# Performance work log

Measured on AMD Instinct MI355X. Metric: run time of the kernel, lower is better.

Reference implementation:

```python
import jax, jax.numpy as jnp
import numpy as np

KP_VARIANCE = 0.01  # init kwarg: kp_variance (float -> plain Gaussian branch)


def make_coordinate_grid(h, w, dtype):
    # torch make_coordinate_grid: x,y in [-1,1], last dim is (x, y)
    x = jnp.linspace(-1.0, 1.0, w, dtype=dtype)
    y = jnp.linspace(-1.0, 1.0, h, dtype=dtype)
    gx, gy = jnp.meshgrid(x, y)  # each (h, w)
    return jnp.stack([gx, gy], axis=-1)  # (h, w, 2)


def grid_sample_bilinear(img, coords):
    """F.grid_sample, bilinear, zeros padding, align_corners=True.
    img: (bs, C, H, W); coords: (bs, d, K, h, w, 2) with (x, y) in [-1,1].
    Returns (bs, d, K, C, h, w)."""
    bs, C, H, W = img.shape
    x = (coords[..., 0] + 1.0) * (W - 1) / 2.0
    y = (coords[..., 1] + 1.0) * (H - 1) / 2.0
    x0 = jnp.floor(x); y0 = jnp.floor(y)
    x1 = x0 + 1.0;     y1 = y0 + 1.0
    wx1 = x - x0; wx0 = 1.0 - wx1
    wy1 = y - y0; wy0 = 1.0 - wy1

    def corner(ix, iy, wgt):
        valid = (ix >= 0) & (ix <= W - 1) & (iy >= 0) & (iy <= H - 1)
        ixc = jnp.clip(ix, 0, W - 1).astype(jnp.int32)
        iyc = jnp.clip(iy, 0, H - 1).astype(jnp.int32)
        # per-batch gather: im (C,H,W), yy/xx (d,K,h,w) -> (C,d,K,h,w)
        vals = jax.vmap(lambda im, yy, xx: im[:, yy, xx])(img, iyc, ixc)  # (bs,C,d,K,h,w)
        w_eff = (wgt * valid.astype(img.dtype))[:, None]  # (bs,1,d,K,h,w)
        return vals * w_eff

    out = (corner(x0, y0, wx0 * wy0) + corner(x1, y0, wx1 * wy0)
           + corner(x0, y1, wx0 * wy1) + corner(x1, y1, wx1 * wy1))
    return jnp.transpose(out, (0, 2, 3, 1, 4, 5))  # (bs,d,K,C,h,w)


def setup_inputs() -> dict:
    key = jax.random.key(0)
    k1, k2, k3 = jax.random.split(key, 3)
    bs, d, K, C, h, w = 4, 16, 10, 3, 128, 128
    kp_appearance_mean = jax.random.uniform(k1, (bs, 1, K, 2), jnp.float32) * 2.0 - 1.0
    kp_video_mean = jax.random.uniform(k2, (bs, d, K, 2), jnp.float32) * 2.0 - 1.0
    appearance_frame = jax.random.normal(k3, (bs, C, 1, h, w), jnp.float32)
    return {"kp_appearance_mean": kp_appearance_mean,
            "kp_video_mean": kp_video_mean,
            "appearance_frame": appearance_frame}


def reference(kp_appearance_mean, kp_video_mean, appearance_frame):
    bs, C, _, h, w = appearance_frame.shape
    _, d, K, _ = kp_video_mean.shape
    dtype = appearance_frame.dtype

    # combine_kp (difference_type='absolute', float kp_variance)
    diff = kp_video_mean - kp_video_mean[:, 0:1]          # (bs,d,K,2)
    kp_mean = diff + kp_appearance_mean                    # (bs,d,K,2)
    kp_video_diff = -diff                                  # (bs,d,K,2)

    grid = make_coordinate_grid(h, w, dtype)               # (h,w,2)

    # use_heatmap: kp2gaussian then subtract first frame
    mean_sub = grid - kp_mean[:, :, :, None, None, :]      # (bs,d,K,h,w,2)
    heatmap = jnp.exp(-0.5 * jnp.sum(mean_sub * mean_sub, axis=-1) / KP_VARIANCE)
    heatmap = heatmap - heatmap[:, 0:1]
    heatmap = heatmap[:, :, :, None]                       # (bs,d,K,1,h,w)

    # use_difference: broadcast diff over spatial dims
    diff_maps = jnp.broadcast_to(kp_video_diff[:, :, :, :, None, None],
                                 (bs, d, K, 2, h, w))

    # use_deformed_appearance: grid_sample of appearance frame by shifted grid
    deformation = grid + kp_video_diff[:, :, :, None, None, :]  # (bs,d,K,h,w,2)
    img = appearance_frame[:, :, 0]                              # (bs,C,h,w)
    deformed = grid_sample_bilinear(img, deformation)            # (bs,d,K,C,h,w)

    enc = jnp.concatenate([heatmap, diff_maps, deformed], axis=3)  # (bs,d,K,1+2+C,h,w)
    enc = enc.reshape(bs, d, -1, h, w)
    return jnp.transpose(enc, (0, 2, 1, 3, 4))  # (bs, (3+C)*K, d, h, w)
```

## Files before the change

kernel.cpp:

```cpp
#include <hip/hip_runtime.h>

#define BS 4
#define DD 16
#define KK 10
#define CC 3
#define HH 128
#define WW 128
#define HW   (HH*WW)
#define CHW  (CC*HW)
#define IMG_FLOATS (BS*CHW)
#define PAD_FLOATS 24576
#define WS_NEED ((size_t)(IMG_FLOATS + 2*PAD_FLOATS) * 4)

using f4 = __attribute__((ext_vector_type(4))) float;

struct F4U { float v[4]; };

__global__ __launch_bounds__(256) void img_pad_copy(
    const float* __restrict__ img, float* __restrict__ dst)
{
    const int i = (int)(blockIdx.x * 256u + threadIdx.x) * 4;
    *(f4*)(dst + i) = *(const f4*)(img + i);
}

template<bool PADDED>
__global__ __launch_bounds__(256) void movement_embed_kernel(
    const float* __restrict__ kp_app,
    const float* __restrict__ kp_vid,
    const float* __restrict__ src,
    float* __restrict__ out)
{
    const unsigned bi  = blockIdx.x;
    const unsigned sub = bi & 15u;
    const unsigned bdk = bi >> 4;
    const unsigned k   = bdk % KK;
    const unsigned t2  = bdk / KK;
    const unsigned d   = t2 % DD;
    const unsigned b   = t2 / DD;

    const int tid = (int)threadIdx.x;
    const int xg  = tid & 31;
    const int ly  = tid >> 5;
    const int x4  = xg * 4;
    const int y   = (int)(sub * 8u) + ly;

    const float kvx  = kp_vid[((b*DD + d)*KK + k)*2 + 0];
    const float kvy  = kp_vid[((b*DD + d)*KK + k)*2 + 1];
    const float kv0x = kp_vid[((b*DD + 0)*KK + k)*2 + 0];
    const float kv0y = kp_vid[((b*DD + 0)*KK + k)*2 + 1];
    const float kax  = kp_app[(b*KK + k)*2 + 0];
    const float kay  = kp_app[(b*KK + k)*2 + 1];

    const float diffx = kvx - kv0x;
    const float diffy = kvy - kv0y;
    const float mx = diffx + kax;
    const float my = diffy + kay;
    const float vdx = -diffx;
    const float vdy = -diffy;

    const float cx = vdx * 63.5f;
    const float cy = vdy * 63.5f;
    const float fcx = floorf(cx), fcy = floorf(cy);
    const int icx = (int)fcx, icy = (int)fcy;
    const float wx1 = cx - fcx, wx0 = 1.0f - wx1;
    const float wy1 = cy - fcy, wy0 = 1.0f - wy1;

    const int r0   = y + icy;
    const int col0 = icx + x4;
    const bool rv0 = (unsigned)r0       < (unsigned)HH;
    const bool rv1 = (unsigned)(r0 + 1) < (unsigned)HH;
    bool cv[5];
#pragma unroll
    for (int e = 0; e < 5; ++e) cv[e] = (unsigned)(col0 + e) < (unsigned)WW;

    const float step = 2.0f / 127.0f;
    const float gy  = (float)y  * step - 1.0f;
    const float gx0 = (float)x4 * step - 1.0f;
    const float dy1 = gy - my, dy0 = gy - kay;
    const float dy1sq = dy1 * dy1, dy0sq = dy0 * dy0;
    float hvv[4];
#pragma unroll
    for (int j = 0; j < 4; ++j) {
        const float gx = gx0 + (float)j * step;
        const float dx1 = gx - mx, dx0 = gx - kax;
        hvv[j] = __expf(-50.0f * (dx1 * dx1 + dy1sq))
               - __expf(-50.0f * (dx0 * dx0 + dy0sq));
    }

    const size_t chs  = (size_t)DD * HW;
    const size_t base = ((((size_t)b * (KK * 6) + k * 6) * DD + d) * HH + y) * WW + (size_t)x4;

    {
        f4 H;  H.x = hvv[0]; H.y = hvv[1]; H.z = hvv[2]; H.w = hvv[3];
        *(f4*)(out + base) = H;
        f4 VX; VX.x = vdx; VX.y = vdx; VX.z = vdx; VX.w = vdx;
        *(f4*)(out + base + chs) = VX;
        f4 VY; VY.x = vdy; VY.y = vdy; VY.z = vdy; VY.w = vdy;
        *(f4*)(out + base + 2 * chs) = VY;
    }

#pragma unroll
    for (int c = 0; c < CC; ++c) {
        float a0[5], a1[5];
        if constexpr (PADDED) {
            const long idx = (long)b * CHW + (long)c * HW + (long)r0 * WW + (long)col0;
            const float* p = src + idx;
            const F4U A  = *(const F4U*)p;
            const float a4 = p[4];
            const F4U Bt = *(const F4U*)(p + WW);
            const float b4 = p[WW + 4];
#pragma unroll
            for (int e = 0; e < 4; ++e) { a0[e] = A.v[e]; a1[e] = Bt.v[e]; }
            a0[4] = a4; a1[4] = b4;
        } else {
            const int rc0 = min(max(r0, 0), HH - 1);
            const int rc1 = min(max(r0 + 1, 0), HH - 1);
            const int cb  = b * CHW + c * HW;
#pragma unroll
            for (int e = 0; e < 5; ++e) {
                const int cc = min(max(col0 + e, 0), WW - 1);
                a0[e] = src[cb + rc0 * WW + cc];
                a1[e] = src[cb + rc1 * WW + cc];
            }
        }
#pragma unroll
        for (int e = 0; e < 5; ++e) {
            a0[e] = (rv0 && cv[e]) ? a0[e] : 0.0f;
            a1[e] = (rv1 && cv[e]) ? a1[e] : 0.0f;
        }
        float dvv[4];
#pragma unroll
        for (int e = 0; e < 4; ++e) {
            const float h0 = wx0 * a0[e] + wx1 * a0[e + 1];
            const float h1 = wx0 * a1[e] + wx1 * a1[e + 1];
            dvv[e] = wy0 * h0 + wy1 * h1;
        }
        f4 DV; DV.x = dvv[0]; DV.y = dvv[1]; DV.z = dvv[2]; DV.w = dvv[3];
        *(f4*)(out + base + (size_t)(3 + c) * chs) = DV;
    }
}

extern "C" void kernel_launch(void* const* d_in, const int* in_sizes, int n_in,
                              void* d_out, int out_size, void* d_ws, size_t ws_size,
                              hipStream_t stream) {
    const float* kp_app = (const float*)d_in[0];
    const float* kp_vid = (const float*)d_in[1];
    const float* img    = (const float*)d_in[2];
    float* out = (float*)d_out;

    const int nblocks = BS * DD * KK * 16;

    if (d_ws != nullptr && ws_size >= WS_NEED) {
        float* wimg = (float*)d_ws;
        img_pad_copy<<<IMG_FLOATS / (256 * 4), 256, 0, stream>>>(img, wimg + PAD_FLOATS);
        movement_embed_kernel<true><<<nblocks, 256, 0, stream>>>(
            kp_app, kp_vid, wimg + PAD_FLOATS, out);
    } else {
        movement_embed_kernel<false><<<nblocks, 256, 0, stream>>>(
            kp_app, kp_vid, img, out);
    }
}
```

Before: 243.9 us.

## Use persistent grid-stride sweep over contiguous output chunks, one channel per chunk

```diff
diff --git a/kernel.cpp b/kernel.cpp
--- a/kernel.cpp
+++ b/kernel.cpp
@@ -12,6 +12,11 @@
 #define PAD_FLOATS 24576
 #define WS_NEED ((size_t)(IMG_FLOATS + 2*PAD_FLOATS) * 4)
 
+#define NCH    (6*KK)
+#define NCHUNK (BS*NCH*DD*16)
+#define NBLK   2048
+#define CPB    (NCHUNK/NBLK)
+
 using f4 = __attribute__((ext_vector_type(4))) float;
 
 struct F4U { float v[4]; };
@@ -24,119 +29,114 @@
 }
 
 template<bool PADDED>
-__global__ __launch_bounds__(256) void movement_embed_kernel(
+__global__ __launch_bounds__(256) void movement_embed_sweep(
     const float* __restrict__ kp_app,
     const float* __restrict__ kp_vid,
     const float* __restrict__ src,
     float* __restrict__ out)
 {
-    const unsigned bi  = blockIdx.x;
-    const unsigned sub = bi & 15u;
-    const unsigned bdk = bi >> 4;
-    const unsigned k   = bdk % KK;
-    const unsigned t2  = bdk / KK;
-    const unsigned d   = t2 % DD;
-    const unsigned b   = t2 / DD;
+    const int tid = (int)threadIdx.x;
+    const int ly  = tid >> 5;
+    const int x4  = (tid & 31) * 4;
+    const float step = 2.0f / 127.0f;
+    const float gx0  = (float)x4 * step - 1.0f;
 
-    const int tid = (int)threadIdx.x;
-    const int xg  = tid & 31;
-    const int ly  = tid >> 5;
-    const int x4  = xg * 4;
-    const int y   = (int)(sub * 8u) + ly;
+    for (int j = (int)blockIdx.x; j < NCHUNK; j += NBLK) {
+        const int sub = j & 15;
+        const int d   = (j >> 4) & 15;
+        const unsigned bc = (unsigned)j >> 8;
+        const unsigned ch = bc % NCH;
+        const unsigned b  = bc / NCH;
+        const unsigned k  = ch / 6u;
+        const unsigned c  = ch - k * 6u;
 
-    const float kvx  = kp_vid[((b*DD + d)*KK + k)*2 + 0];
-    const float kvy  = kp_vid[((b*DD + d)*KK + k)*2 + 1];
-    const float kv0x = kp_vid[((b*DD + 0)*KK + k)*2 + 0];
-    const float kv0y = kp_vid[((b*DD + 0)*KK + k)*2 + 1];
-    const float kax  = kp_app[(b*KK + k)*2 + 0];
-    const float kay  = kp_app[(b*KK + k)*2 + 1];
+        const int y = sub * 8 + ly;
 
-    const float diffx = kvx - kv0x;
-    const float diffy = kvy - kv0y;
-    const float mx = diffx + kax;
-    const float my = diffy + kay;
-    const float vdx = -diffx;
-    const float vdy = -diffy;
+        const float kvx  = kp_vid[((b*DD + d)*KK + k)*2 + 0];
+        const float kvy  = kp_vid[((b*DD + d)*KK + k)*2 + 1];
+        const float kv0x = kp_vid[((b*DD + 0)*KK + k)*2 + 0];
+        const float kv0y = kp_vid[((b*DD + 0)*KK + k)*2 + 1];
+        const float kax  = kp_app[(b*KK + k)*2 + 0];
+        const float kay  = kp_app[(b*KK + k)*2 + 1];
 
-    const float cx = vdx * 63.5f;
-    const float cy = vdy * 63.5f;
-    const float fcx = floorf(cx), fcy = floorf(cy);
-    const int icx = (int)fcx, icy = (int)fcy;
-    const float wx1 = cx - fcx, wx0 = 1.0f - wx1;
-    const float wy1 = cy - fcy, wy0 = 1.0f - wy1;
+        const float diffx = kvx - kv0x;
+        const float diffy = kvy - kv0y;
+        const float vdx = -diffx;
+        const float vdy = -diffy;
 
-    const int r0   = y + icy;
-    const int col0 = icx + x4;
-    const bool rv0 = (unsigned)r0       < (unsigned)HH;
-    const bool rv1 = (unsigned)(r0 + 1) < (unsigned)HH;
-    bool cv[5];
+        f4 V;
+        if (c == 0) {
+            const float mx = diffx + kax;
+            const float my = diffy + kay;
+            const float gy  = (float)y * step - 1.0f;
+            const float dy1 = gy - my, dy0 = gy - kay;
+            const float dy1sq = dy1 * dy1, dy0sq = dy0 * dy0;
+            float hv[4];
 #pragma unroll
-    for (int e = 0; e < 5; ++e) cv[e] = (unsigned)(col0 + e) < (unsigned)WW;
+            for (int e = 0; e < 4; ++e) {
+                const float gx = gx0 + (float)e * step;
+                const float dx1 = gx - mx, dx0 = gx - kax;
+                hv[e] = __expf(-50.0f * (dx1 * dx1 + dy1sq))
+                      - __expf(-50.0f * (dx0 * dx0 + dy0sq));
+            }
+            V.x = hv[0]; V.y = hv[1]; V.z = hv[2]; V.w = hv[3];
+        } else if (c == 1) {
+            V.x = vdx; V.y = vdx; V.z = vdx; V.w = vdx;
+        } else if (c == 2) {
+            V.x = vdy; V.y = vdy; V.z = vdy; V.w = vdy;
+        } else {
+            const float cx = vdx * 63.5f;
+            const float cy = vdy * 63.5f;
+            const float fcx = floorf(cx), fcy = floorf(cy);
+            const int icx = (int)fcx, icy = (int)fcy;
+            const float wx1 = cx - fcx, wx0 = 1.0f - wx1;
+            const float wy1 = cy - fcy, wy0 = 1.0f - wy1;
 
-    const float step = 2.0f / 127.0f;
-    const float gy  = (float)y  * step - 1.0f;
-    const float gx0 = (float)x4 * step - 1.0f;
-    const float dy1 = gy - my, dy0 = gy - kay;
-    const float dy1sq = dy1 * dy1, dy0sq = dy0 * dy0;
-    float hvv[4];
+            const int r0   = y + icy;
+            const int col0 = icx + x4;
+            const bool rv0 = (unsigned)r0       < (unsigned)HH;
+            const bool rv1 = (unsigned)(r0 + 1) < (unsigned)HH;
+
+            float a0[5], a1[5];
+            if constexpr (PADDED) {
+                const long idx = (long)b * CHW + (long)(c - 3u) * HW
+                               + (long)r0 * WW + (long)col0;
+                const float* p = src + idx;
+                const F4U A  = *(const F4U*)p;
+                const float a4 = p[4];
+                const F4U Bt = *(const F4U*)(p + WW);
+                const float b4 = p[WW + 4];
 #pragma unroll
-    for (int j = 0; j < 4; ++j) {
-        const float gx = gx0 + (float)j * step;
-        const float dx1 = gx - mx, dx0 = gx - kax;
-        hvv[j] = __expf(-50.0f * (dx1 * dx1 + dy1sq))
-               - __expf(-50.0f * (dx0 * dx0 + dy0sq));
-    }
-
-    const size_t chs  = (size_t)DD * HW;
-    const size_t base = ((((size_t)b * (KK * 6) + k * 6) * DD + d) * HH + y) * WW + (size_t)x4;
-
-    {
-        f4 H;  H.x = hvv[0]; H.y = hvv[1]; H.z = hvv[2]; H.w = hvv[3];
-        *(f4*)(out + base) = H;
-        f4 VX; VX.x = vdx; VX.y = vdx; VX.z = vdx; VX.w = vdx;
-        *(f4*)(out + base + chs) = VX;
-        f4 VY; VY.x = vdy; VY.y = vdy; VY.z = vdy; VY.w = vdy;
-        *(f4*)(out + base + 2 * chs) = VY;
-    }
-
+                for (int e = 0; e < 4; ++e) { a0[e] = A.v[e]; a1[e] = Bt.v[e]; }
+                a0[4] = a4; a1[4] = b4;
+            } else {
+                const int rc0 = min(max(r0, 0), HH - 1);
+                const int rc1 = min(max(r0 + 1, 0), HH - 1);
+                const int cb  = (int)b * CHW + (int)(c - 3u) * HW;
 #pragma unroll
-    for (int c = 0; c < CC; ++c) {
-        float a0[5], a1[5];
-        if constexpr (PADDED) {
-            const long idx = (long)b * CHW + (long)c * HW + (long)r0 * WW + (long)col0;
-            const float* p = src + idx;
-            const F4U A  = *(const F4U*)p;
-            const float a4 = p[4];
-            const F4U Bt = *(const F4U*)(p + WW);
-            const float b4 = p[WW + 4];
-#pragma unroll
-            for (int e = 0; e < 4; ++e) { a0[e] = A.v[e]; a1[e] = Bt.v[e]; }
-            a0[4] = a4; a1[4] = b4;
-        } else {
-            const int rc0 = min(max(r0, 0), HH - 1);
-            const int rc1 = min(max(r0 + 1, 0), HH - 1);
-            const int cb  = b * CHW + c * HW;
+                for (int e = 0; e < 5; ++e) {
+                    const int cc = min(max(col0 + e, 0), WW - 1);
+                    a0[e] = src[cb + rc0 * WW + cc];
+                    a1[e] = src[cb + rc1 * WW + cc];
+                }
+            }
 #pragma unroll
             for (int e = 0; e < 5; ++e) {
-                const int cc = min(max(col0 + e, 0), WW - 1);
-                a0[e] = src[cb + rc0 * WW + cc];
-                a1[e] = src[cb + rc1 * WW + cc];
+                const bool cvv = (unsigned)(col0 + e) < (unsigned)WW;
+                a0[e] = (rv0 && cvv) ? a0[e] : 0.0f;
+                a1[e] = (rv1 && cvv) ? a1[e] : 0.0f;
             }
+            float dv[4];
+#pragma unroll
+            for (int e = 0; e < 4; ++e) {
+                const float h0 = wx0 * a0[e] + wx1 * a0[e + 1];
+                const float h1 = wx0 * a1[e] + wx1 * a1[e + 1];
+                dv[e] = wy0 * h0 + wy1 * h1;
+            }
+            V.x = dv[0]; V.y = dv[1]; V.z = dv[2]; V.w = dv[3];
         }
-#pragma unroll
-        for (int e = 0; e < 5; ++e) {
-            a0[e] = (rv0 && cv[e]) ? a0[e] : 0.0f;
-            a1[e] = (rv1 && cv[e]) ? a1[e] : 0.0f;
-        }
-        float dvv[4];
-#pragma unroll
-        for (int e = 0; e < 4; ++e) {
-            const float h0 = wx0 * a0[e] + wx1 * a0[e + 1];
-            const float h1 = wx0 * a1[e] + wx1 * a1[e + 1];
-            dvv[e] = wy0 * h0 + wy1 * h1;
-        }
-        f4 DV; DV.x = dvv[0]; DV.y = dvv[1]; DV.z = dvv[2]; DV.w = dvv[3];
-        *(f4*)(out + base + (size_t)(3 + c) * chs) = DV;
+
+        *(f4*)(out + ((size_t)(unsigned)j << 10) + (unsigned)(tid << 2)) = V;
     }
 }
 
@@ -148,15 +148,13 @@
     const float* img    = (const float*)d_in[2];
     float* out = (float*)d_out;
 
-    const int nblocks = BS * DD * KK * 16;
-
     if (d_ws != nullptr && ws_size >= WS_NEED) {
         float* wimg = (float*)d_ws;
         img_pad_copy<<<IMG_FLOATS / (256 * 4), 256, 0, stream>>>(img, wimg + PAD_FLOATS);
-        movement_embed_kernel<true><<<nblocks, 256, 0, stream>>>(
+        movement_embed_sweep<true><<<NBLK, 256, 0, stream>>>(
             kp_app, kp_vid, wimg + PAD_FLOATS, out);
     } else {
-        movement_embed_kernel<false><<<nblocks, 256, 0, stream>>>(
+        movement_embed_sweep<false><<<NBLK, 256, 0, stream>>>(
             kp_app, kp_vid, img, out);
     }
 }
```

Result: slower. 251.1 us (+2.9%).
